# Kernel tuning notes

Measured on AMD Instinct MI355X. Metric: run time of the kernel, lower is better.

## Reference

```python
import jax, jax.numpy as jnp
import numpy as np

N = 100000   # nodes
E = 1600000  # edges (avg degree 16)
D = 32       # feature dim

def setup_inputs() -> dict:
    key = jax.random.key(0)
    k1, k2, k3, k4 = jax.random.split(key, 4)
    feat = jax.random.normal(k1, (N, D), dtype=jnp.float32)
    e_feat = jax.random.normal(k2, (E, 1), dtype=jnp.float32)
    src = jax.random.randint(k3, (E,), 0, N)
    dst = jax.random.randint(k4, (E,), 0, N)
    return {"feat": feat, "e_feat": e_feat, "src": src, "dst": dst}

def reference(feat, e_feat, src, dst):
    n = feat.shape[0]
    ones = jnp.ones(src.shape[0], dtype=feat.dtype)
    # degrees computed on the full graph (before self-loop removal), as in DGL code
    out_deg = jax.ops.segment_sum(ones, src, num_segments=n)
    in_deg = jax.ops.segment_sum(ones, dst, num_segments=n)
    src_norm = jnp.power(jnp.clip(out_deg, 1.0, None), -0.5)[:, None]  # [N,1]
    dst_norm = jnp.power(jnp.clip(in_deg, 1.0, None), -0.5)[:, None]   # [N,1]
    # remove_self_loop: mask out self-loop edges in the aggregation only
    mask = (src != dst).astype(feat.dtype)[:, None]                    # [E,1]
    # u_mul_e: gather normalized src features, multiply by edge weight
    msg = (feat * src_norm)[src] * (e_feat * mask)                     # [E,D]
    agg = jax.ops.segment_sum(msg, dst, num_segments=n)                # [N,D]
    out = feat - agg * dst_norm
    return jnp.sum(jnp.abs(out), axis=1)                               # [N]
```

## Files before the change

kernel.cpp:

```cpp
#include <hip/hip_runtime.h>

#define D 32
#define RANGE 128
#define RMAX 800
#define JC 512
#define CHUNKMAX 3200
#define CAP 2304

__global__ __launch_bounds__(512) void sort_chunks(
        const int* __restrict__ src, const int* __restrict__ dst,
        const float* __restrict__ ef,
        uint2* __restrict__ recs, unsigned* __restrict__ recsS,
        unsigned* __restrict__ metaD, unsigned* __restrict__ metaS,
        int E, int R, int chunk) {
    __shared__ uint2 sd[CHUNKMAX];
    __shared__ unsigned ss_[CHUNKMAX];
    __shared__ int cd[RMAX], cs[RMAX];
    __shared__ int curD[RMAX], curS[RMAX];
    int j = blockIdx.x, t = threadIdx.x;
    int e0 = j * chunk, e1 = min(E, e0 + chunk), cntE = e1 - e0;
    for (int i = t; i < RMAX; i += 512) { cd[i] = 0; cs[i] = 0; }
    __syncthreads();
    for (int e = e0 + 2 * t; e < e1; e += 1024) {
        if (e + 1 < e1) {
            int2 s2 = *(const int2*)(src + e);
            int2 d2 = *(const int2*)(dst + e);
            atomicAdd(&cd[d2.x >> 7], 1);
            atomicAdd(&cd[d2.y >> 7], 1);
            atomicAdd(&cs[s2.x >> 7], 1);
            atomicAdd(&cs[s2.y >> 7], 1);
        } else {
            atomicAdd(&cd[dst[e] >> 7], 1);
            atomicAdd(&cs[src[e] >> 7], 1);
        }
    }
    __syncthreads();
    {
        int i1 = t + 512;
        curD[t] = cd[t]; curS[t] = cs[t];
        if (i1 < RMAX) { curD[i1] = cd[i1]; curS[i1] = cs[i1]; }
        __syncthreads();
        for (int off = 1; off < RMAX; off <<= 1) {
            int vD0 = (t >= off) ? curD[t - off] : 0;
            int vS0 = (t >= off) ? curS[t - off] : 0;
            int vD1 = 0, vS1 = 0;
            if (i1 < RMAX && i1 >= off) { vD1 = curD[i1 - off]; vS1 = curS[i1 - off]; }
            __syncthreads();
            curD[t] += vD0; curS[t] += vS0;
            if (i1 < RMAX) { curD[i1] += vD1; curS[i1] += vS1; }
            __syncthreads();
        }
        curD[t] -= cd[t]; curS[t] -= cs[t];
        if (i1 < RMAX) { curD[i1] -= cd[i1]; curS[i1] -= cs[i1]; }
        __syncthreads();
    }
    for (int e = e0 + t; e < e1; e += 512) {
        int s = src[e], d = dst[e];
        float w = (s == d) ? 0.0f : ef[e];
        int pos = atomicAdd(&curD[d >> 7], 1);
        sd[pos] = make_uint2((unsigned)s | ((unsigned)(d & (RANGE - 1)) << 17),
                             __float_as_uint(w));
        int ps = atomicAdd(&curS[s >> 7], 1);
        ss_[ps] = (unsigned)s;
    }
    __syncthreads();
    size_t baseE = (size_t)j * chunk;
    for (int i = t; i < cntE; i += 512) {
        recs[baseE + i] = sd[i];
        recsS[baseE + i] = ss_[i];
    }
    for (int i = t; i < R; i += 512) {
        metaD[(size_t)j * R + i] = ((unsigned)(curD[i] - cd[i]) << 16) | (unsigned)cd[i];
        metaS[(size_t)j * R + i] = ((unsigned)(curS[i] - cs[i]) << 16) | (unsigned)cs[i];
    }
}

__device__ __forceinline__ unsigned short f2bf(float x) {
    unsigned u = __float_as_uint(x);
    u += 0x7FFFu + ((u >> 16) & 1u);
    return (unsigned short)(u >> 16);
}

__global__ __launch_bounds__(512) void srcnorm_convert(
        const unsigned* __restrict__ recsS, const unsigned* __restrict__ metaS,
        const float* __restrict__ feat, unsigned short* __restrict__ featb,
        int n, int R, int chunk) {
    __shared__ int cnt[RANGE];
    int r = blockIdx.x, t = threadIdx.x;
    int base = r * RANGE, lim = min(n - base, RANGE);
    if (t < RANGE) cnt[t] = 0;
    __syncthreads();
    unsigned m = metaS[(size_t)t * R + r];
    int st = m >> 16, c = m & 0xFFFFu;
    const unsigned* p = recsS + (size_t)t * chunk + st;
    for (int k = 0; k < c; k++) atomicAdd(&cnt[p[k] - (unsigned)base], 1);
    __syncthreads();
    int total4 = lim * 8;
    for (int i = t; i < total4; i += 512) {
        int row = i >> 3;
        float sn = rsqrtf((float)max(cnt[row], 1));
        float4 f = ((const float4*)(feat + (size_t)(base + row) * D))[i & 7];
        ushort4 u;
        u.x = f2bf(f.x * sn); u.y = f2bf(f.y * sn);
        u.z = f2bf(f.z * sn); u.w = f2bf(f.w * sn);
        ((ushort4*)(featb + (size_t)(base + row) * D))[i & 7] = u;
    }
}

__global__ __launch_bounds__(512) void gather_kernel(
        const float* __restrict__ feat, const unsigned short* __restrict__ featb,
        const uint2* __restrict__ recs, const unsigned* __restrict__ metaD,
        float* __restrict__ out, int n, int R, int chunk) {
    __shared__ uint2 raw[CAP];
    __shared__ uint2 srec[CAP];
    __shared__ int segpre[JC + 1];
    __shared__ int indeg[RANGE];
    __shared__ int pre[RANGE + 1];
    int r = blockIdx.x, t = threadIdx.x;
    int base = r * RANGE, lim = min(n - base, RANGE);
    unsigned m = metaD[(size_t)t * R + r];
    int st = m >> 16, c = m & 0xFFFFu;
    segpre[t + 1] = c;
    if (t == 0) segpre[0] = 0;
    if (t < RANGE) indeg[t] = 0;
    __syncthreads();
    for (int off = 1; off < JC; off <<= 1) {
        int v = (t + 1 > off) ? segpre[t + 1 - off] : 0;
        __syncthreads();
        segpre[t + 1] += v;
        __syncthreads();
    }
    int total = segpre[JC];
    bool ovf = total > CAP;
    const uint2* p = recs + (size_t)t * chunk + st;
    if (!ovf) {
        int dp = segpre[t];
        for (int k = 0; k < c; k++) {
            uint2 rec = p[k];
            raw[dp + k] = rec;
            atomicAdd(&indeg[rec.x >> 17], 1);
        }
    } else {
        for (int k = 0; k < c; k++) atomicAdd(&indeg[p[k].x >> 17], 1);
    }
    __syncthreads();
    if (t < RANGE) pre[t + 1] = indeg[t];
    if (t == 0) pre[0] = 0;
    __syncthreads();
    for (int off = 1; off < RANGE; off <<= 1) {
        int v = 0;
        if (t < RANGE) { int idx = t + 1; if (idx > off) v = pre[idx - off]; }
        __syncthreads();
        if (t < RANGE) pre[t + 1] += v;
        __syncthreads();
    }
    if (t < RANGE) indeg[t] = pre[t];
    __syncthreads();
    if (!ovf) {
        for (int i = t; i < total; i += 512) {
            uint2 rec = raw[i];
            int dl = rec.x >> 17;
            int pos = atomicAdd(&indeg[dl], 1);
            srec[pos] = make_uint2(rec.x & 0x1FFFFu, rec.y);
        }
    }
    __syncthreads();
    int node = t >> 2;
    int cch = t & 3;
    if (node >= lim) return;
    int p0i = pre[node];
    int cnt = pre[node + 1] - p0i;
    float a0 = 0.f, a1 = 0.f, a2 = 0.f, a3 = 0.f, a4 = 0.f, a5 = 0.f, a6 = 0.f, a7 = 0.f;
    if (!ovf) {
        const uint2* sp = srec + p0i;
        int i = 0;
        for (; i + 4 <= cnt; i += 4) {
            uint2 q0 = sp[i], q1 = sp[i + 1], q2 = sp[i + 2], q3 = sp[i + 3];
            uint4 b0 = ((const uint4*)(featb + (size_t)q0.x * D))[cch];
            uint4 b1 = ((const uint4*)(featb + (size_t)q1.x * D))[cch];
            uint4 b2 = ((const uint4*)(featb + (size_t)q2.x * D))[cch];
            uint4 b3 = ((const uint4*)(featb + (size_t)q3.x * D))[cch];
            float w0 = __uint_as_float(q0.y), w1 = __uint_as_float(q1.y);
            float w2 = __uint_as_float(q2.y), w3 = __uint_as_float(q3.y);
            a0 += __uint_as_float(b0.x << 16) * w0 + __uint_as_float(b1.x << 16) * w1
                + __uint_as_float(b2.x << 16) * w2 + __uint_as_float(b3.x << 16) * w3;
            a1 += __uint_as_float(b0.x & 0xFFFF0000u) * w0 + __uint_as_float(b1.x & 0xFFFF0000u) * w1
                + __uint_as_float(b2.x & 0xFFFF0000u) * w2 + __uint_as_float(b3.x & 0xFFFF0000u) * w3;
            a2 += __uint_as_float(b0.y << 16) * w0 + __uint_as_float(b1.y << 16) * w1
                + __uint_as_float(b2.y << 16) * w2 + __uint_as_float(b3.y << 16) * w3;
            a3 += __uint_as_float(b0.y & 0xFFFF0000u) * w0 + __uint_as_float(b1.y & 0xFFFF0000u) * w1
                + __uint_as_float(b2.y & 0xFFFF0000u) * w2 + __uint_as_float(b3.y & 0xFFFF0000u) * w3;
            a4 += __uint_as_float(b0.z << 16) * w0 + __uint_as_float(b1.z << 16) * w1
                + __uint_as_float(b2.z << 16) * w2 + __uint_as_float(b3.z << 16) * w3;
            a5 += __uint_as_float(b0.z & 0xFFFF0000u) * w0 + __uint_as_float(b1.z & 0xFFFF0000u) * w1
                + __uint_as_float(b2.z & 0xFFFF0000u) * w2 + __uint_as_float(b3.z & 0xFFFF0000u) * w3;
            a6 += __uint_as_float(b0.w << 16) * w0 + __uint_as_float(b1.w << 16) * w1
                + __uint_as_float(b2.w << 16) * w2 + __uint_as_float(b3.w << 16) * w3;
            a7 += __uint_as_float(b0.w & 0xFFFF0000u) * w0 + __uint_as_float(b1.w & 0xFFFF0000u) * w1
                + __uint_as_float(b2.w & 0xFFFF0000u) * w2 + __uint_as_float(b3.w & 0xFFFF0000u) * w3;
        }
        for (; i < cnt; i++) {
            uint2 q = sp[i];
            uint4 b = ((const uint4*)(featb + (size_t)q.x * D))[cch];
            float w = __uint_as_float(q.y);
            a0 += __uint_as_float(b.x << 16) * w;
            a1 += __uint_as_float(b.x & 0xFFFF0000u) * w;
            a2 += __uint_as_float(b.y << 16) * w;
            a3 += __uint_as_float(b.y & 0xFFFF0000u) * w;
            a4 += __uint_as_float(b.z << 16) * w;
            a5 += __uint_as_float(b.z & 0xFFFF0000u) * w;
            a6 += __uint_as_float(b.w << 16) * w;
            a7 += __uint_as_float(b.w & 0xFFFF0000u) * w;
        }
    } else {
        for (int j = 0; j < JC; j++) {
            unsigned mm = metaD[(size_t)j * R + r];
            const uint2* pp = recs + (size_t)j * chunk + (mm >> 16);
            int cc = mm & 0xFFFFu;
            for (int k = 0; k < cc; k++) {
                uint2 rec = pp[k];
                if ((int)(rec.x >> 17) == node) {
                    uint4 b = ((const uint4*)(featb + (size_t)(rec.x & 0x1FFFFu) * D))[cch];
                    float w = __uint_as_float(rec.y);
                    a0 += __uint_as_float(b.x << 16) * w;
                    a1 += __uint_as_float(b.x & 0xFFFF0000u) * w;
                    a2 += __uint_as_float(b.y << 16) * w;
                    a3 += __uint_as_float(b.y & 0xFFFF0000u) * w;
                    a4 += __uint_as_float(b.z << 16) * w;
                    a5 += __uint_as_float(b.z & 0xFFFF0000u) * w;
                    a6 += __uint_as_float(b.w << 16) * w;
                    a7 += __uint_as_float(b.w & 0xFFFF0000u) * w;
                }
            }
        }
    }
    float dn = rsqrtf((float)max(cnt, 1));
    const float4* fr = (const float4*)(feat + (size_t)(base + node) * D);
    float4 fA = fr[cch * 2];
    float4 fB = fr[cch * 2 + 1];
    float v = fabsf(fA.x - a0 * dn) + fabsf(fA.y - a1 * dn) +
              fabsf(fA.z - a2 * dn) + fabsf(fA.w - a3 * dn) +
              fabsf(fB.x - a4 * dn) + fabsf(fB.y - a5 * dn) +
              fabsf(fB.z - a6 * dn) + fabsf(fB.w - a7 * dn);
    v += __shfl_xor(v, 1, 4);
    v += __shfl_xor(v, 2, 4);
    if (cch == 0) out[base + node] = v;
}

extern "C" void kernel_launch(void* const* d_in, const int* in_sizes, int n_in,
                              void* d_out, int out_size, void* d_ws, size_t ws_size,
                              hipStream_t stream) {
    const float* feat   = (const float*)d_in[0];
    const float* e_feat = (const float*)d_in[1];
    const int*   src    = (const int*)d_in[2];
    const int*   dst    = (const int*)d_in[3];
    const int E = in_sizes[2];
    const int n = in_sizes[0] / D;
    float* out = (float*)d_out;

    const int R = (n + RANGE - 1) / RANGE;
    const int chunk = (((E + JC - 1) / JC) + 1) & ~1;

    char* p = (char*)d_ws;
    uint2* recs    = (uint2*)p;    p += ((size_t)JC * chunk * 8 + 15) & ~(size_t)15;
    unsigned* recsS = (unsigned*)p; p += ((size_t)JC * chunk * 4 + 15) & ~(size_t)15;
    unsigned* metaD = (unsigned*)p; p += ((size_t)JC * R * 4 + 15) & ~(size_t)15;
    unsigned* metaS = (unsigned*)p; p += ((size_t)JC * R * 4 + 15) & ~(size_t)15;
    unsigned short* featb = (unsigned short*)p;

    sort_chunks<<<JC, 512, 0, stream>>>(src, dst, e_feat, recs, recsS, metaD, metaS,
                                        E, R, chunk);

    srcnorm_convert<<<R, 512, 0, stream>>>(recsS, metaS, feat, featb, n, R, chunk);

    gather_kernel<<<R, 512, 0, stream>>>(feat, featb, recs, metaD, out, n, R, chunk);
}
```

Measured before the change: 145.3 us.

## Compute out-degree with global atomics instead of sorting source records

The source-bucket sort (recsS, metaS and their shared-memory histograms and scans) is dropped. Out-degree is now counted with one global atomicAdd per edge into a zeroed array, and srcnorm_convert becomes a flat elementwise pass. This removes a 4-byte-per-edge write plus its re-read, and halves the shared-memory scan work in sort_chunks. metaD is also transposed so gather_kernel reads it contiguously. The cost is 1.6M scattered global atomics plus an extra zeroing launch.

```diff
diff --git a/kernel.cpp b/kernel.cpp
--- a/kernel.cpp
+++ b/kernel.cpp
@@ -7,72 +7,66 @@
 #define CHUNKMAX 3200
 #define CAP 2304
 
+__global__ __launch_bounds__(256) void zero_outdeg(int4* __restrict__ outdeg4, int n4) {
+    int i = blockIdx.x * 256 + threadIdx.x;
+    if (i < n4) outdeg4[i] = make_int4(0, 0, 0, 0);
+}
+
 __global__ __launch_bounds__(512) void sort_chunks(
         const int* __restrict__ src, const int* __restrict__ dst,
         const float* __restrict__ ef,
-        uint2* __restrict__ recs, unsigned* __restrict__ recsS,
-        unsigned* __restrict__ metaD, unsigned* __restrict__ metaS,
+        uint2* __restrict__ recs, unsigned* __restrict__ metaD,
+        int* __restrict__ outdeg,
         int E, int R, int chunk) {
     __shared__ uint2 sd[CHUNKMAX];
-    __shared__ unsigned ss_[CHUNKMAX];
-    __shared__ int cd[RMAX], cs[RMAX];
-    __shared__ int curD[RMAX], curS[RMAX];
+    __shared__ int cd[RMAX];
+    __shared__ int curD[RMAX];
     int j = blockIdx.x, t = threadIdx.x;
     int e0 = j * chunk, e1 = min(E, e0 + chunk), cntE = e1 - e0;
-    for (int i = t; i < RMAX; i += 512) { cd[i] = 0; cs[i] = 0; }
+    for (int i = t; i < RMAX; i += 512) cd[i] = 0;
     __syncthreads();
     for (int e = e0 + 2 * t; e < e1; e += 1024) {
         if (e + 1 < e1) {
-            int2 s2 = *(const int2*)(src + e);
             int2 d2 = *(const int2*)(dst + e);
             atomicAdd(&cd[d2.x >> 7], 1);
             atomicAdd(&cd[d2.y >> 7], 1);
-            atomicAdd(&cs[s2.x >> 7], 1);
-            atomicAdd(&cs[s2.y >> 7], 1);
         } else {
             atomicAdd(&cd[dst[e] >> 7], 1);
-            atomicAdd(&cs[src[e] >> 7], 1);
         }
     }
     __syncthreads();
     {
         int i1 = t + 512;
-        curD[t] = cd[t]; curS[t] = cs[t];
-        if (i1 < RMAX) { curD[i1] = cd[i1]; curS[i1] = cs[i1]; }
+        curD[t] = cd[t];
+        if (i1 < RMAX) curD[i1] = cd[i1];
         __syncthreads();
         for (int off = 1; off < RMAX; off <<= 1) {
-            int vD0 = (t >= off) ? curD[t - off] : 0;
-            int vS0 = (t >= off) ? curS[t - off] : 0;
-            int vD1 = 0, vS1 = 0;
-            if (i1 < RMAX && i1 >= off) { vD1 = curD[i1 - off]; vS1 = curS[i1 - off]; }
+            int v0 = (t >= off) ? curD[t - off] : 0;
+            int v1 = 0;
+            if (i1 < RMAX && i1 >= off) v1 = curD[i1 - off];
             __syncthreads();
-            curD[t] += vD0; curS[t] += vS0;
-            if (i1 < RMAX) { curD[i1] += vD1; curS[i1] += vS1; }
+            curD[t] += v0;
+            if (i1 < RMAX) curD[i1] += v1;
             __syncthreads();
         }
-        curD[t] -= cd[t]; curS[t] -= cs[t];
-        if (i1 < RMAX) { curD[i1] -= cd[i1]; curS[i1] -= cs[i1]; }
+        curD[t] -= cd[t];
+        if (i1 < RMAX) curD[i1] -= cd[i1];
         __syncthreads();
     }
     for (int e = e0 + t; e < e1; e += 512) {
         int s = src[e], d = dst[e];
         float w = (s == d) ? 0.0f : ef[e];
+        atomicAdd(&outdeg[s], 1);
         int pos = atomicAdd(&curD[d >> 7], 1);
         sd[pos] = make_uint2((unsigned)s | ((unsigned)(d & (RANGE - 1)) << 17),
                              __float_as_uint(w));
-        int ps = atomicAdd(&curS[s >> 7], 1);
-        ss_[ps] = (unsigned)s;
     }
     __syncthreads();
     size_t baseE = (size_t)j * chunk;
-    for (int i = t; i < cntE; i += 512) {
-        recs[baseE + i] = sd[i];
-        recsS[baseE + i] = ss_[i];
-    }
-    for (int i = t; i < R; i += 512) {
-        metaD[(size_t)j * R + i] = ((unsigned)(curD[i] - cd[i]) << 16) | (unsigned)cd[i];
-        metaS[(size_t)j * R + i] = ((unsigned)(curS[i] - cs[i]) << 16) | (unsigned)cs[i];
-    }
+    for (int i = t; i < cntE; i += 512) recs[baseE + i] = sd[i];
+    for (int i = t; i < R; i += 512)
+        metaD[(size_t)i * JC + j] =
+            ((unsigned)(curD[i] - cd[i]) << 16) | (unsigned)cd[i];
 }
 
 __device__ __forceinline__ unsigned short f2bf(float x) {
@@ -81,30 +75,19 @@
     return (unsigned short)(u >> 16);
 }
 
-__global__ __launch_bounds__(512) void srcnorm_convert(
-        const unsigned* __restrict__ recsS, const unsigned* __restrict__ metaS,
-        const float* __restrict__ feat, unsigned short* __restrict__ featb,
-        int n, int R, int chunk) {
-    __shared__ int cnt[RANGE];
-    int r = blockIdx.x, t = threadIdx.x;
-    int base = r * RANGE, lim = min(n - base, RANGE);
-    if (t < RANGE) cnt[t] = 0;
-    __syncthreads();
-    unsigned m = metaS[(size_t)t * R + r];
-    int st = m >> 16, c = m & 0xFFFFu;
-    const unsigned* p = recsS + (size_t)t * chunk + st;
-    for (int k = 0; k < c; k++) atomicAdd(&cnt[p[k] - (unsigned)base], 1);
-    __syncthreads();
-    int total4 = lim * 8;
-    for (int i = t; i < total4; i += 512) {
-        int row = i >> 3;
-        float sn = rsqrtf((float)max(cnt[row], 1));
-        float4 f = ((const float4*)(feat + (size_t)(base + row) * D))[i & 7];
-        ushort4 u;
-        u.x = f2bf(f.x * sn); u.y = f2bf(f.y * sn);
-        u.z = f2bf(f.z * sn); u.w = f2bf(f.w * sn);
-        ((ushort4*)(featb + (size_t)(base + row) * D))[i & 7] = u;
-    }
+__global__ __launch_bounds__(256) void srcnorm_convert(
+        const int* __restrict__ outdeg, const float* __restrict__ feat,
+        unsigned short* __restrict__ featb, int n) {
+    int i = blockIdx.x * 256 + threadIdx.x;
+    int total = n * 8;
+    if (i >= total) return;
+    int row = i >> 3;
+    float sn = rsqrtf((float)max(outdeg[row], 1));
+    float4 f = ((const float4*)feat)[i];
+    ushort4 u;
+    u.x = f2bf(f.x * sn); u.y = f2bf(f.y * sn);
+    u.z = f2bf(f.z * sn); u.w = f2bf(f.w * sn);
+    ((ushort4*)featb)[i] = u;
 }
 
 __global__ __launch_bounds__(512) void gather_kernel(
@@ -118,7 +101,7 @@
     __shared__ int pre[RANGE + 1];
     int r = blockIdx.x, t = threadIdx.x;
     int base = r * RANGE, lim = min(n - base, RANGE);
-    unsigned m = metaD[(size_t)t * R + r];
+    unsigned m = metaD[(size_t)r * JC + t];
     int st = m >> 16, c = m & 0xFFFFu;
     segpre[t + 1] = c;
     if (t == 0) segpre[0] = 0;
@@ -214,7 +197,7 @@
         }
     } else {
         for (int j = 0; j < JC; j++) {
-            unsigned mm = metaD[(size_t)j * R + r];
+            unsigned mm = metaD[(size_t)r * JC + j];
             const uint2* pp = recs + (size_t)j * chunk + (mm >> 16);
             int cc = mm & 0xFFFFu;
             for (int k = 0; k < cc; k++) {
@@ -262,16 +245,19 @@
     const int chunk = (((E + JC - 1) / JC) + 1) & ~1;
 
     char* p = (char*)d_ws;
-    uint2* recs    = (uint2*)p;    p += ((size_t)JC * chunk * 8 + 15) & ~(size_t)15;
-    unsigned* recsS = (unsigned*)p; p += ((size_t)JC * chunk * 4 + 15) & ~(size_t)15;
-    unsigned* metaD = (unsigned*)p; p += ((size_t)JC * R * 4 + 15) & ~(size_t)15;
-    unsigned* metaS = (unsigned*)p; p += ((size_t)JC * R * 4 + 15) & ~(size_t)15;
+    uint2* recs     = (uint2*)p;    p += ((size_t)JC * chunk * 8 + 15) & ~(size_t)15;
+    unsigned* metaD = (unsigned*)p; p += ((size_t)R * JC * 4 + 15) & ~(size_t)15;
+    int* outdeg     = (int*)p;
+    const int n4 = (n + 3) / 4;
+    p += ((size_t)n4 * 16 + 15) & ~(size_t)15;
     unsigned short* featb = (unsigned short*)p;
 
-    sort_chunks<<<JC, 512, 0, stream>>>(src, dst, e_feat, recs, recsS, metaD, metaS,
+    zero_outdeg<<<(n4 + 255) / 256, 256, 0, stream>>>((int4*)outdeg, n4);
+
+    sort_chunks<<<JC, 512, 0, stream>>>(src, dst, e_feat, recs, metaD, outdeg,
                                         E, R, chunk);
 
-    srcnorm_convert<<<R, 512, 0, stream>>>(recsS, metaS, feat, featb, n, R, chunk);
+    srcnorm_convert<<<(n * 8 + 255) / 256, 256, 0, stream>>>(outdeg, feat, featb, n);
 
     gather_kernel<<<R, 512, 0, stream>>>(feat, featb, recs, metaD, out, n, R, chunk);
 }
```

Result: slower. 189.7 us (+30.5%).
